# Optimization experiments

Measured on AMD Instinct MI355X. Metric: run time of the kernel, lower is better.

## Reference

```python
import jax, jax.numpy as jnp
import numpy as np

D_MODEL = 512; D_STATE = 128; D_CONV = 4; EXPAND = 2; HEADDIM = 64; CHUNK = 64
D_INNER = EXPAND * D_MODEL            # 1024
NHEADS = D_INNER // HEADDIM           # 16
CONV_DIM = D_INNER + 2 * D_STATE      # 1280
D_IN_PROJ = 2 * D_INNER + 2 * D_STATE + NHEADS  # 2320
BATCH, SEQLEN = 2, 8192


def setup_inputs() -> dict:
    key = jax.random.key(0)
    ks = jax.random.split(key, 8)
    s = 0.02
    return {
        "x": jax.random.normal(ks[0], (BATCH, SEQLEN, D_MODEL), jnp.float32),
        "in_proj_w": jax.random.normal(ks[1], (D_IN_PROJ, D_MODEL), jnp.float32) * s,
        "conv_w": jax.random.normal(ks[2], (CONV_DIM, 1, D_CONV), jnp.float32) * s,
        "conv_b": jnp.zeros((CONV_DIM,), jnp.float32),
        "dt_bias": jax.random.normal(ks[3], (NHEADS,), jnp.float32) * s,
        "A_log": jnp.log(jnp.arange(1, NHEADS + 1, dtype=jnp.float32)),
        "D_skip": jnp.ones((NHEADS,), jnp.float32),
        "norm_w": jnp.ones((D_INNER,), jnp.float32),
        "ssm_out_w": jax.random.normal(ks[4], (D_MODEL, D_INNER), jnp.float32) * s,
        "fuse_w": jax.random.normal(ks[5], (D_MODEL, 2 * D_MODEL), jnp.float32) * s,
        "fuse_b": jnp.zeros((D_MODEL,), jnp.float32),
    }


def segsum(a):
    # a: (..., T) -> (..., T, T) with [i, j] = sum_{j < d <= i} a[d]; -inf above diag
    T = a.shape[-1]
    a = jnp.broadcast_to(a[..., :, None], a.shape + (T,))
    a = jnp.where(jnp.tril(jnp.ones((T, T), bool), -1), a, 0.0)
    a = jnp.cumsum(a, axis=-2)
    return jnp.where(jnp.tril(jnp.ones((T, T), bool), 0), a, -jnp.inf)


def ssd(x, A, B, C):
    # x: (b,l,h,p), A: (b,l,h), B/C: (b,l,n) (single group, broadcast over heads)
    b, l, h, p = x.shape
    c = l // CHUNK
    x = x.reshape(b, c, CHUNK, h, p)
    A = jnp.transpose(A.reshape(b, c, CHUNK, h), (0, 3, 1, 2))   # (b,h,c,s)
    B = B.reshape(b, c, CHUNK, -1)
    C = C.reshape(b, c, CHUNK, -1)
    A_cumsum = jnp.cumsum(A, axis=-1)                             # (b,h,c,s)
    L = jnp.exp(segsum(A))                                        # (b,h,c,s,s) intra-chunk decay
    Y_diag = jnp.einsum("bcln,bcsn,bhcls,bcshp->bclhp", C, B, L, x)
    decay_states = jnp.exp(A_cumsum[..., -1:] - A_cumsum)         # (b,h,c,s)
    states = jnp.einsum("bcln,bhcl,bclhp->bchpn", B, decay_states, x)
    init = jnp.zeros_like(states[:, :1])
    A_pad = jnp.pad(A_cumsum[..., -1], ((0, 0), (0, 0), (1, 0)))  # (b,h,c+1)
    decay_chunk = jnp.exp(segsum(A_pad))                          # (b,h,c+1,c+1)
    new_states = jnp.einsum("bhzc,bchpn->bzhpn", decay_chunk,
                            jnp.concatenate([init, states], axis=1))
    states = new_states[:, :-1]                                   # state entering each chunk
    state_decay_out = jnp.exp(A_cumsum)
    Y_off = jnp.einsum("bchpn,bcsn,bhcs->bcshp", states, C, state_decay_out)
    return (Y_diag + Y_off).reshape(b, l, h, p)


def mamba2_block(u, in_proj_w, conv_w, conv_b, dt_bias, A_log, D_skip, norm_w, ssm_out_w):
    b, l, _ = u.shape
    zxbcdt = u @ in_proj_w.T                                      # (b,l,2320)
    z = zxbcdt[..., :D_INNER]
    xBC = zxbcdt[..., D_INNER:D_INNER + CONV_DIM]
    dt = jax.nn.softplus(zxbcdt[..., -NHEADS:] + dt_bias)         # (b,l,h)
    # depthwise causal conv over time
    conv = jax.lax.conv_general_dilated(
        jnp.transpose(xBC, (0, 2, 1)), conv_w, (1,), [(D_CONV - 1, 0)],
        dimension_numbers=("NCH", "OIH", "NCH"), feature_group_count=CONV_DIM)
    xBC = jax.nn.silu(jnp.transpose(conv + conv_b[None, :, None], (0, 2, 1)))
    xh = xBC[..., :D_INNER].reshape(b, l, NHEADS, HEADDIM)
    Bm = xBC[..., D_INNER:D_INNER + D_STATE]
    Cm = xBC[..., -D_STATE:]
    A = -jnp.exp(A_log)                                           # (h,)
    y = ssd(xh * dt[..., None], A * dt, Bm, Cm)
    y = y + xh * D_skip[None, None, :, None]
    y = y.reshape(b, l, D_INNER)
    # gated RMSNorm
    y = y * jax.nn.silu(z)
    y = y * jax.lax.rsqrt(jnp.mean(y * y, axis=-1, keepdims=True) + 1e-5) * norm_w
    return y @ ssm_out_w.T


def reference(x, in_proj_w, conv_w, conv_b, dt_bias, A_log, D_skip, norm_w,
              ssm_out_w, fuse_w, fuse_b):
    args = (in_proj_w, conv_w, conv_b, dt_bias, A_log, D_skip, norm_w, ssm_out_w)
    y_fwd = mamba2_block(x, *args)
    y_rev = jnp.flip(mamba2_block(jnp.flip(x, 1), *args), 1)
    y_cat = jnp.concatenate([y_fwd, y_rev], axis=-1)
    return y_cat @ fuse_w.T + fuse_b
```

## Files before the change

### kernel.cpp

```cpp
#include <hip/hip_runtime.h>
#include <cstddef>

#define B_SZ     2
#define L_SEQ    8192
#define D_INNERC 1024
#define NHEADSC  16
#define CHUNKC   64
#define NCHUNKC  128
#define CONV_DIMC 1280
#define D_PROJC  2320
#define M_ROWS   16384

typedef unsigned short bfu;

using bf16x8 = __attribute__((ext_vector_type(8))) short;
using f32x4  = __attribute__((ext_vector_type(4))) float;

__device__ __forceinline__ float silu_(float v) { return v / (1.f + expf(-v)); }

__device__ __forceinline__ float b2f(bfu u) {
  return __uint_as_float((unsigned)u << 16);
}
__device__ __forceinline__ bfu f2b(float f) {
  unsigned x = __float_as_uint(f);
  return (bfu)((x + 0x7fffu + ((x >> 16) & 1u)) >> 16);
}

__device__ __forceinline__ float4 ld4(const float* p) { return *(const float4*)p; }
__device__ __forceinline__ float4 ld4(const bfu* p) {
  ushort4 u = *(const ushort4*)p;
  float4 f;
  f.x = b2f(u.x); f.y = b2f(u.y); f.z = b2f(u.z); f.w = b2f(u.w);
  return f;
}
__device__ __forceinline__ void st4(float* p, float4 v) { *(float4*)p = v; }
__device__ __forceinline__ void st4(bfu* p, float4 v) {
  ushort4 u;
  u.x = f2b(v.x); u.y = f2b(v.y); u.z = f2b(v.z); u.w = f2b(v.w);
  *(ushort4*)p = u;
}

__device__ __forceinline__ void gl_lds16(const bfu* g, bfu* l) {
  __builtin_amdgcn_global_load_lds(
      (const __attribute__((address_space(1))) unsigned int*)g,
      (__attribute__((address_space(3))) unsigned int*)l, 16, 0, 0);
}

__device__ __forceinline__ int pos_of(int b, int c, int l, int dir) {
  int t = c * CHUNKC + l;
  return dir ? (b * L_SEQ + (L_SEQ - 1) - t) : (b * L_SEQ + t);
}

__global__ __launch_bounds__(256)
void mfma_nt(const bfu* __restrict__ A, int lda,
             const bfu* __restrict__ Bw, int ldb,
             void* __restrict__ Cv, int ldc,
             int N, int K, const float* __restrict__ bias, int mode)
{
  __shared__ bfu sh[16384];
  bfu* As = sh;
  bfu* Bs = sh + 8192;
  const int tid  = threadIdx.x;
  const int lane = tid & 63;
  const int wave = __builtin_amdgcn_readfirstlane(tid >> 6);
  const int wm = wave & 1, wn = wave >> 1;

  const int num_n = gridDim.x;
  const int flat  = blockIdx.y * num_n + blockIdx.x;
  const int xcd   = flat & 7;
  const int g     = flat >> 3;
  const int n0 = (g % num_n) * 128;
  const int m0 = ((g / num_n) * 8 + xcd) * 128;

  f32x4 acc[4][4];
#pragma unroll
  for (int i = 0; i < 4; ++i)
#pragma unroll
    for (int j = 0; j < 4; ++j)
      acc[i][j] = (f32x4){0.f, 0.f, 0.f, 0.f};

  const int ro   = lane >> 3;
  const int slot = lane & 7;

  for (int k0 = 0; k0 < K; k0 += 64) {
    __syncthreads();
#pragma unroll
    for (int si = 0; si < 4; ++si) {
      int r = wave * 32 + si * 8 + ro;
      int cg = slot ^ (r & 7);
      gl_lds16(A  + (size_t)(m0 + r) * lda + k0 + cg * 8, As + (wave * 32 + si * 8) * 64);
      gl_lds16(Bw + (size_t)(n0 + r) * ldb + k0 + cg * 8, Bs + (wave * 32 + si * 8) * 64);
    }
    __syncthreads();

#pragma unroll
    for (int ks = 0; ks < 2; ++ks) {
      bf16x8 af[4], bfr[4];
#pragma unroll
      for (int i = 0; i < 4; ++i) {
        int ra = wm * 64 + i * 16 + (lane & 15);
        int ca = (ks * 4 + (lane >> 4)) ^ (ra & 7);
        af[i] = *(const bf16x8*)(As + ra * 64 + ca * 8);
        int rb = wn * 64 + i * 16 + (lane & 15);
        int cb = (ks * 4 + (lane >> 4)) ^ (rb & 7);
        bfr[i] = *(const bf16x8*)(Bs + rb * 64 + cb * 8);
      }
#pragma unroll
      for (int i = 0; i < 4; ++i)
#pragma unroll
        for (int j = 0; j < 4; ++j)
          acc[i][j] = __builtin_amdgcn_mfma_f32_16x16x32_bf16(af[i], bfr[j], acc[i][j], 0, 0, 0);
    }
  }

  __syncthreads();
  if (mode == 0) {
#pragma unroll
    for (int i = 0; i < 4; ++i)
#pragma unroll
      for (int j = 0; j < 4; ++j)
#pragma unroll
        for (int r = 0; r < 4; ++r) {
          int ml = wm * 64 + i * 16 + (lane >> 4) * 4 + r;
          int nl = wn * 64 + j * 16 + (lane & 15);
          sh[ml * 128 + nl] = f2b(acc[i][j][r]);
        }
    __syncthreads();
    bfu* Cb = (bfu*)Cv;
#pragma unroll
    for (int rr = 0; rr < 8; ++rr) {
      int idx = rr * 256 + tid;
      int row = idx >> 4, co = (idx & 15) * 8;
      if (n0 + co < N) {
        *(ulonglong2*)(Cb + (size_t)(m0 + row) * ldc + n0 + co) =
            *(const ulonglong2*)(sh + row * 128 + co);
      }
    }
  } else {
    float* Cf = (float*)Cv;
    float* shf = (float*)sh;
#pragma unroll
    for (int p = 0; p < 2; ++p) {
      if (wm == p) {
#pragma unroll
        for (int i = 0; i < 4; ++i)
#pragma unroll
          for (int j = 0; j < 4; ++j)
#pragma unroll
            for (int r = 0; r < 4; ++r) {
              int ml = i * 16 + (lane >> 4) * 4 + r;
              int nl = wn * 64 + j * 16 + (lane & 15);
              shf[ml * 128 + nl] = acc[i][j][r];
            }
      }
      __syncthreads();
#pragma unroll
      for (int rr = 0; rr < 8; ++rr) {
        int idx = rr * 256 + tid;
        int row = idx >> 5, co = (idx & 31) * 4;
        int n = n0 + co;
        if (n < N) {
          float4 v = *(float4*)(shf + row * 128 + co);
          float* cp = Cf + (size_t)(m0 + p * 64 + row) * ldc + n;
          if (mode == 2) {
            float4 o = *(float4*)cp;
            v.x += o.x; v.y += o.y; v.z += o.z; v.w += o.w;
          } else if (bias) {
            v.x += bias[n]; v.y += bias[n + 1]; v.z += bias[n + 2]; v.w += bias[n + 3];
          }
          *(float4*)cp = v;
        }
      }
      __syncthreads();
    }
  }
}

__global__ __launch_bounds__(512)
void mfma_nt_8p(const bfu* __restrict__ A, int lda,
                const bfu* __restrict__ Bw, int ldb,
                bfu* __restrict__ C, int ldc, int N, int K)
{
  __shared__ bfu sh[65536];
  bfu* As0 = sh;
  bfu* As1 = sh + 16384;
  bfu* Bs0 = sh + 32768;
  bfu* Bs1 = sh + 49152;

  const int tid  = threadIdx.x;
  const int lane = tid & 63;
  const int w    = __builtin_amdgcn_readfirstlane(tid >> 6);
  const int wm = w & 1, wn = w >> 1;
  const int q = lane >> 4, t = lane & 15;

  const int num_n = gridDim.x;
  const int flat  = blockIdx.y * num_n + blockIdx.x;
  const int xcd   = flat & 7;
  const int g     = flat >> 3;
  const int n0 = (g % num_n) * 256;
  const int m0 = ((g / num_n) * 8 + xcd) * 256;

  auto STG = [&](const bfu* __restrict__ X, int ldx, int x0, int kt, int h,
                 bfu* dst) {
#pragma unroll
    for (int ci = 0; ci < 2; ++ci) {
      int rb = h * 128 + ci * 64 + w * 8;
      int r  = rb + (lane >> 3);
      int cg = (lane & 7) ^ (r & 7);
      gl_lds16(X + (size_t)(x0 + r) * ldx + kt * 64 + cg * 8, dst + rb * 64);
    }
  };
  auto FR = [&](const bfu* tile, int R, int gg) -> bf16x8 {
    return *(const bf16x8*)(tile + R * 64 + ((gg ^ (R & 7)) * 8));
  };

  f32x4 acc[8][4];
#pragma unroll
  for (int i = 0; i < 8; ++i)
#pragma unroll
    for (int j = 0; j < 4; ++j)
      acc[i][j] = (f32x4){0.f, 0.f, 0.f, 0.f};

  STG(Bw, ldb, n0, 0, 0, Bs0); STG(Bw, ldb, n0, 0, 1, Bs0);
  STG(A,  lda, m0, 0, 0, As0); STG(A,  lda, m0, 0, 1, As0);
  STG(Bw, ldb, n0, 1, 0, Bs1); STG(Bw, ldb, n0, 1, 1, Bs1);
  asm volatile("s_waitcnt vmcnt(4)" ::: "memory");
  __builtin_amdgcn_s_barrier();

  const int nIter = K >> 7;
  bf16x8 bfr[4][2];
  for (int it = 0; it < nIter; ++it) {
    const int kt = it * 2;
    const bool last = (it == nIter - 1);

#pragma unroll
    for (int p = 0; p < 4; ++p) {
      bf16x8 af[2][2];
#pragma unroll
      for (int ii = 0; ii < 2; ++ii)
#pragma unroll
        for (int ks = 0; ks < 2; ++ks)
          af[ii][ks] = FR(As0, wm * 128 + (2 * p + ii) * 16 + t, ks * 4 + q);
      if (p == 0) {
#pragma unroll
        for (int j = 0; j < 4; ++j)
#pragma unroll
          for (int ks = 0; ks < 2; ++ks)
            bfr[j][ks] = FR(Bs0, wn * 64 + j * 16 + t, ks * 4 + q);
      }
      if (p == 0)          STG(A,  lda, m0, kt + 1, 0, As1);
      if (p == 1)          STG(A,  lda, m0, kt + 1, 1, As1);
      if (p == 2 && !last) STG(Bw, ldb, n0, kt + 2, 0, Bs0);
      if (p == 3 && !last) STG(Bw, ldb, n0, kt + 2, 1, Bs0);
      if (p == 3) {
        if (last) asm volatile("s_waitcnt vmcnt(0)" ::: "memory");
        else      asm volatile("s_waitcnt vmcnt(4)" ::: "memory");
      }
      __builtin_amdgcn_s_barrier();
      __builtin_amdgcn_s_setprio(1);
#pragma unroll
      for (int ks = 0; ks < 2; ++ks)
#pragma unroll
        for (int ii = 0; ii < 2; ++ii)
#pragma unroll
          for (int j = 0; j < 4; ++j)
            acc[2 * p + ii][j] = __builtin_amdgcn_mfma_f32_16x16x32_bf16(
                af[ii][ks], bfr[j][ks], acc[2 * p + ii][j], 0, 0, 0);
      __builtin_amdgcn_s_setprio(0);
      __builtin_amdgcn_s_barrier();
    }

#pragma unroll
    for (int p = 0; p < 4; ++p) {
      bf16x8 af[2][2];
#pragma unroll
      for (int ii = 0; ii < 2; ++ii)
#pragma unroll
        for (int ks = 0; ks < 2; ++ks)
          af[ii][ks] = FR(As1, wm * 128 + (2 * p + ii) * 16 + t, ks * 4 + q);
      if (p == 0) {
#pragma unroll
        for (int j = 0; j < 4; ++j)
#pragma unroll
          for (int ks = 0; ks < 2; ++ks)
            bfr[j][ks] = FR(Bs1, wn * 64 + j * 16 + t, ks * 4 + q);
      }
      if (p == 0 && !last) STG(A,  lda, m0, kt + 2, 0, As0);
      if (p == 1 && !last) STG(A,  lda, m0, kt + 2, 1, As0);
      if (p == 2 && !last) STG(Bw, ldb, n0, kt + 3, 0, Bs1);
      if (p == 3 && !last) STG(Bw, ldb, n0, kt + 3, 1, Bs1);
      if (p == 3 && !last) asm volatile("s_waitcnt vmcnt(4)" ::: "memory");
      __builtin_amdgcn_s_barrier();
      __builtin_amdgcn_s_setprio(1);
#pragma unroll
      for (int ks = 0; ks < 2; ++ks)
#pragma unroll
        for (int ii = 0; ii < 2; ++ii)
#pragma unroll
          for (int j = 0; j < 4; ++j)
            acc[2 * p + ii][j] = __builtin_amdgcn_mfma_f32_16x16x32_bf16(
                af[ii][ks], bfr[j][ks], acc[2 * p + ii][j], 0, 0, 0);
      __builtin_amdgcn_s_setprio(0);
      __builtin_amdgcn_s_barrier();
    }
  }

#pragma unroll
  for (int i = 0; i < 8; ++i)
#pragma unroll
    for (int j = 0; j < 4; ++j)
#pragma unroll
      for (int r = 0; r < 4; ++r) {
        int ml = wm * 128 + i * 16 + q * 4 + r;
        int nl = wn * 64 + j * 16 + t;
        sh[ml * 256 + nl] = f2b(acc[i][j][r]);
      }
  __syncthreads();
#pragma unroll
  for (int rr = 0; rr < 16; ++rr) {
    int idx = rr * 512 + tid;
    int row = idx >> 5, co = (idx & 31) * 8;
    if (n0 + co < N) {
      *(ulonglong2*)(C + (size_t)(m0 + row) * ldc + n0 + co) =
          *(const ulonglong2*)(sh + row * 256 + co);
    }
  }
}

__global__ __launch_bounds__(256)
void cvt_x_k(const float* __restrict__ in, bfu* __restrict__ out)
{
  int q = blockIdx.x * 256 + threadIdx.x;
  st4(out + (size_t)q * 4, ld4(in + (size_t)q * 4));
}

__global__ __launch_bounds__(256)
void cvt_w_k(const float* __restrict__ in, bfu* __restrict__ out)
{
  int q = blockIdx.x * 256 + threadIdx.x;
  int row = q >> 7, c4 = (q & 127) << 2;
  float4 v = {0.f, 0.f, 0.f, 0.f};
  if (row < D_PROJC) v = ld4(in + (size_t)row * 512 + c4);
  st4(out + (size_t)row * 512 + c4, v);
}

__global__ __launch_bounds__(256)
void transpose_k(const float* __restrict__ in, bfu* __restrict__ out)
{
  int idx = blockIdx.x * 256 + threadIdx.x;
  int j = idx >> 9, k = idx & 511;
  out[idx] = f2b(in[k * 1024 + j]);
}

__global__ __launch_bounds__(256)
void cvt_fuse_k(const float* __restrict__ in, bfu* __restrict__ out)
{
  int q = blockIdx.x * 256 + threadIdx.x;
  int m = q >> 7, kg = (q & 127) << 2;
  float4 v = ld4(in + (size_t)(m & 511) * 1024 + (m >> 9) * 512 + kg);
  st4(out + (size_t)m * 512 + kg, v);
}

__global__ __launch_bounds__(256)
void conv_k(const bfu* __restrict__ zx, const float* __restrict__ conv_w,
            const float* __restrict__ conv_b, bfu* __restrict__ xBC, int dir)
{
  int ch = blockIdx.x * 256 + threadIdx.x;
  int m0 = blockIdx.y * 8;
  int b  = m0 >> 13, tb = m0 & (L_SEQ - 1);
  float w0 = conv_w[ch * 4 + 0], w1 = conv_w[ch * 4 + 1];
  float w2 = conv_w[ch * 4 + 2], w3 = conv_w[ch * 4 + 3];
  float cb = conv_b[ch];
  const bfu* src = zx + 1024 + ch;
  const int shift = dir ? 0 : 3;

  float v[11];
#pragma unroll
  for (int i = 0; i < 11; ++i) {
    int tt = tb + i - shift;
    v[i] = (tt >= 0 && tt < L_SEQ)
         ? b2f(src[(size_t)(b * L_SEQ + tt) * D_PROJC]) : 0.f;
  }
#pragma unroll
  for (int j = 0; j < 8; ++j) {
    float acc = cb;
    if (dir == 0) {
      acc += w0 * v[j] + w1 * v[j + 1] + w2 * v[j + 2] + w3 * v[j + 3];
    } else {
      acc += w0 * v[j + 3] + w1 * v[j + 2] + w2 * v[j + 1] + w3 * v[j];
    }
    xBC[(size_t)(m0 + j) * CONV_DIMC + ch] = f2b(silu_(acc));
  }
}

__global__ __launch_bounds__(256)
void states_mfma_k(const bfu* __restrict__ zx, const bfu* __restrict__ xBC,
                   const float* __restrict__ dt_bias, const float* __restrict__ A_log,
                   float* __restrict__ acum_g, float* __restrict__ dt_g,
                   bfu* __restrict__ states, int dir)
{
  __shared__ bfu BT[128 * 72];
  __shared__ bfu xsT[64 * 72];
  __shared__ float scaleS[8 * 64];

  int bid = blockIdx.x;
  int hb = bid >> 8;
  int c = bid & 127, b = (bid >> 7) & 1;
  int tid = threadIdx.x, lane = tid & 63;
  int w = tid >> 6, q = lane >> 4, t = lane & 15;

#pragma unroll
  for (int rr = 0; rr < 2; ++rr) {
    int i = w + rr * 4;
    int h = hb * 8 + i;
    int l = lane;
    int pos = pos_of(b, c, l, dir);
    float dtr = b2f(zx[(size_t)pos * D_PROJC + 2304 + h]) + dt_bias[h];
    float dt = (dtr > 20.f) ? dtr : log1pf(expf(dtr));
    float a = -expf(A_log[h]) * dt;
#pragma unroll
    for (int off = 1; off < 64; off <<= 1) {
      float v = __shfl_up(a, off);
      if (l >= off) a += v;
    }
    float alast = __shfl(a, 63);
    int gi = ((b * NCHUNKC + c) * NHEADSC + h) * 64 + l;
    acum_g[gi] = a; dt_g[gi] = dt;
    scaleS[i * 64 + l] = dt * expf(alast - a);
  }

#pragma unroll
  for (int r = 0; r < 8; ++r) {
    int qq = tid + r * 256;
    int l = qq & 63, ng = qq >> 6;
    ushort4 v = *(const ushort4*)(xBC + (size_t)pos_of(b, c, l, dir) * CONV_DIMC + 1024 + ng * 4);
    BT[(ng * 4 + 0) * 72 + l] = v.x; BT[(ng * 4 + 1) * 72 + l] = v.y;
    BT[(ng * 4 + 2) * 72 + l] = v.z; BT[(ng * 4 + 3) * 72 + l] = v.w;
  }
  __syncthreads();

  for (int i = 0; i < 8; ++i) {
    int h = hb * 8 + i;
#pragma unroll
    for (int r = 0; r < 4; ++r) {
      int qq = tid + r * 256;
      int l = qq & 63, pg = qq >> 6;
      float s = scaleS[i * 64 + l];
      ushort4 v = *(const ushort4*)(xBC + (size_t)pos_of(b, c, l, dir) * CONV_DIMC + h * 64 + pg * 4);
      xsT[(pg * 4 + 0) * 72 + l] = f2b(b2f(v.x) * s);
      xsT[(pg * 4 + 1) * 72 + l] = f2b(b2f(v.y) * s);
      xsT[(pg * 4 + 2) * 72 + l] = f2b(b2f(v.z) * s);
      xsT[(pg * 4 + 3) * 72 + l] = f2b(b2f(v.w) * s);
    }
    __syncthreads();

    bf16x8 axs[2];
#pragma unroll
    for (int ks = 0; ks < 2; ++ks)
      axs[ks] = *(const bf16x8*)(xsT + (w * 16 + t) * 72 + ks * 32 + q * 8);

    f32x4 acc[8];
#pragma unroll
    for (int j = 0; j < 8; ++j) acc[j] = (f32x4){0.f, 0.f, 0.f, 0.f};
#pragma unroll
    for (int ks = 0; ks < 2; ++ks)
#pragma unroll
      for (int j = 0; j < 8; ++j) {
        bf16x8 bB = *(const bf16x8*)(BT + (j * 16 + t) * 72 + ks * 32 + q * 8);
        acc[j] = __builtin_amdgcn_mfma_f32_16x16x32_bf16(axs[ks], bB, acc[j], 0, 0, 0);
      }

    size_t base = ((size_t)(b * NCHUNKC + c) * NHEADSC + h) * 8192;
#pragma unroll
    for (int j = 0; j < 8; ++j)
#pragma unroll
      for (int r = 0; r < 4; ++r) {
        int p = w * 16 + q * 4 + r, n = j * 16 + t;
        states[base + p * 128 + n] = f2b(acc[j][r]);
      }
    __syncthreads();
  }
}

__global__ __launch_bounds__(256)
void scan_k(bfu* __restrict__ states, const float* __restrict__ acum_g)
{
  int bid = blockIdx.x;
  int eb = bid & 15, h = (bid >> 4) & 15, b = bid >> 8;
  int e = eb * 512 + threadIdx.x * 2;
  bfu* p0 = states + ((size_t)(b * NCHUNKC) * NHEADSC + h) * 8192 + e;
  const float* ac = acum_g + ((b * NCHUNKC) * NHEADSC + h) * 64 + 63;
  const size_t cstride = (size_t)NHEADSC * 8192;
  const int astride = NHEADSC * 64;

  float pre0 = 0.f, pre1 = 0.f;
  uint raw = *(const uint*)p0;
  float dcur = expf(ac[0]);
  for (int c = 0; c < NCHUNKC; ++c) {
    uint raw_next = 0; float dnext = 0.f;
    if (c < NCHUNKC - 1) {
      raw_next = *(const uint*)(p0 + (c + 1) * cstride);
      dnext = expf(ac[(c + 1) * astride]);
    }
    float v0 = b2f((bfu)(raw & 0xffff));
    float v1 = b2f((bfu)(raw >> 16));
    uint packed = (uint)f2b(pre0) | ((uint)f2b(pre1) << 16);
    *(uint*)(p0 + c * cstride) = packed;
    pre0 = v0 + dcur * pre0;
    pre1 = v1 + dcur * pre1;
    raw = raw_next; dcur = dnext;
  }
}

__global__ __launch_bounds__(256)
void y_mfma_k(const bfu* __restrict__ xBC, const bfu* __restrict__ states,
              const float* __restrict__ acum_g, const float* __restrict__ dt_g,
              const float* __restrict__ D_skip, bfu* __restrict__ ybuf, int dir)
{
  __shared__ bfu smem[30976];
  bfu* Cs  = smem;
  bfu* Bsc = smem + 8704;
  bfu* Ps  = smem + 17408;
  bfu* xhT = smem + 26112;
  float* acumH = (float*)(smem + 30720);
  float* dtH   = acumH + 64;

  int bid = blockIdx.x;
  int hb = bid >> 8;
  int c = bid & 127, b = (bid >> 7) & 1;
  int tid = threadIdx.x, lane = tid & 63;
  int w = tid >> 6, q = lane >> 4, t = lane & 15;

#pragma unroll
  for (int r = 0; r < 8; ++r) {
    int qq = tid + r * 256;
    int row = qq >> 5, grp = qq & 31;
    const bfu* src = xBC + (size_t)pos_of(b, c, row, dir) * CONV_DIMC;
    *(ushort4*)(Cs  + row * 136 + grp * 4) = *(const ushort4*)(src + 1152 + grp * 4);
    *(ushort4*)(Bsc + row * 136 + grp * 4) = *(const ushort4*)(src + 1024 + grp * 4);
  }
  __syncthreads();

  bf16x8 af[4];
#pragma unroll
  for (int ks = 0; ks < 4; ++ks)
    af[ks] = *(const bf16x8*)(Cs + (w * 16 + t) * 136 + ks * 32 + q * 8);

  f32x4 sacc[4];
#pragma unroll
  for (int j = 0; j < 4; ++j) sacc[j] = (f32x4){0.f, 0.f, 0.f, 0.f};
#pragma unroll
  for (int ks = 0; ks < 4; ++ks)
#pragma unroll
    for (int j = 0; j < 4; ++j) {
      bf16x8 bf = *(const bf16x8*)(Bsc + (j * 16 + t) * 136 + ks * 32 + q * 8);
      sacc[j] = __builtin_amdgcn_mfma_f32_16x16x32_bf16(af[ks], bf, sacc[j], 0, 0, 0);
    }

  for (int i = 0; i < 8; ++i) {
    int h = hb * 8 + i;
    __syncthreads();
    size_t pbase = ((size_t)(b * NCHUNKC + c) * NHEADSC + h) * 8192;
#pragma unroll
    for (int r = 0; r < 8; ++r) {
      int qq = tid + r * 256;
      int row = qq >> 5, grp = qq & 31;
      *(ushort4*)(Ps + row * 136 + grp * 4) =
          *(const ushort4*)(states + pbase + row * 128 + grp * 4);
    }
#pragma unroll
    for (int r = 0; r < 4; ++r) {
      int qq = tid + r * 256;
      int l = qq & 63, pg = qq >> 6;
      ushort4 v = *(const ushort4*)(xBC + (size_t)pos_of(b, c, l, dir) * CONV_DIMC + h * 64 + pg * 4);
      xhT[(pg * 4 + 0) * 72 + l] = v.x; xhT[(pg * 4 + 1) * 72 + l] = v.y;
      xhT[(pg * 4 + 2) * 72 + l] = v.z; xhT[(pg * 4 + 3) * 72 + l] = v.w;
    }
    if (tid < 64) {
      int gi = ((b * NCHUNKC + c) * NHEADSC + h) * 64 + tid;
      acumH[tid] = acum_g[gi]; dtH[tid] = dt_g[gi];
    }
    __syncthreads();

    f32x4 yacc[4];
#pragma unroll
    for (int j = 0; j < 4; ++j) yacc[j] = (f32x4){0.f, 0.f, 0.f, 0.f};
#pragma unroll
    for (int ks = 0; ks < 4; ++ks)
#pragma unroll
      for (int j = 0; j < 4; ++j) {
        bf16x8 bP = *(const bf16x8*)(Ps + (j * 16 + t) * 136 + ks * 32 + q * 8);
        yacc[j] = __builtin_amdgcn_mfma_f32_16x16x32_bf16(af[ks], bP, yacc[j], 0, 0, 0);
      }

    float Dh = D_skip[h];
    bfu* sc = Bsc;
#pragma unroll
    for (int j = 0; j < 4; ++j)
#pragma unroll
      for (int r = 0; r < 4; ++r) {
        int l = w * 16 + q * 4 + r, s = j * 16 + t;
        float v = 0.f;
        if (s <= l) v = sacc[j][r] * expf(acumH[l] - acumH[s]) * dtH[s];
        if (s == l) v += Dh;
        sc[l * 72 + s] = f2b(v);
      }

    f32x4 acc2[4];
    float dec[4];
#pragma unroll
    for (int r = 0; r < 4; ++r) dec[r] = expf(acumH[w * 16 + q * 4 + r]);
#pragma unroll
    for (int j = 0; j < 4; ++j)
#pragma unroll
      for (int r = 0; r < 4; ++r) acc2[j][r] = yacc[j][r] * dec[r];

#pragma unroll
    for (int ks = 0; ks < 2; ++ks) {
      bf16x8 asc = *(const bf16x8*)(sc + (w * 16 + t) * 72 + ks * 32 + q * 8);
#pragma unroll
      for (int j = 0; j < 4; ++j) {
        bf16x8 bx = *(const bf16x8*)(xhT + (j * 16 + t) * 72 + ks * 32 + q * 8);
        acc2[j] = __builtin_amdgcn_mfma_f32_16x16x32_bf16(asc, bx, acc2[j], 0, 0, 0);
      }
    }

#pragma unroll
    for (int j = 0; j < 4; ++j)
#pragma unroll
      for (int r = 0; r < 4; ++r) {
        int l = w * 16 + q * 4 + r, p = j * 16 + t;
        ybuf[(size_t)pos_of(b, c, l, dir) * D_INNERC + h * 64 + p] = f2b(acc2[j][r]);
      }
  }
}

__global__ __launch_bounds__(256)
void norm_k(bfu* __restrict__ ybuf, const bfu* __restrict__ zx,
            const float* __restrict__ norm_w)
{
  int m = blockIdx.x, tid = threadIdx.x;
  float4 y = ld4(ybuf + (size_t)m * D_INNERC + tid * 4);
  float4 z = ld4(zx + (size_t)m * D_PROJC + tid * 4);
  float4 g;
  g.x = y.x * silu_(z.x); g.y = y.y * silu_(z.y);
  g.z = y.z * silu_(z.z); g.w = y.w * silu_(z.w);
  float ss = g.x * g.x + g.y * g.y + g.z * g.z + g.w * g.w;
#pragma unroll
  for (int off = 32; off >= 1; off >>= 1) ss += __shfl_xor(ss, off);
  __shared__ float red[4];
  int wid = tid >> 6;
  if ((tid & 63) == 0) red[wid] = ss;
  __syncthreads();
  float tot = red[0] + red[1] + red[2] + red[3];
  float scale = rsqrtf(tot * (1.f / 1024.f) + 1e-5f);
  float4 w = *(const float4*)(norm_w + tid * 4);
  g.x *= scale * w.x; g.y *= scale * w.y; g.z *= scale * w.z; g.w *= scale * w.w;
  st4(ybuf + (size_t)m * D_INNERC + tid * 4, g);
}

extern "C" void kernel_launch(void* const* d_in, const int* in_sizes, int n_in,
                              void* d_out, int out_size, void* d_ws, size_t ws_size,
                              hipStream_t stream)
{
  const float* x         = (const float*)d_in[0];
  const float* in_proj_w = (const float*)d_in[1];
  const float* conv_w    = (const float*)d_in[2];
  const float* conv_b    = (const float*)d_in[3];
  const float* dt_bias   = (const float*)d_in[4];
  const float* A_log     = (const float*)d_in[5];
  const float* D_skip    = (const float*)d_in[6];
  const float* norm_w    = (const float*)d_in[7];
  const float* ssm_out_w = (const float*)d_in[8];
  const float* fuse_w    = (const float*)d_in[9];
  const float* fuse_b    = (const float*)d_in[10];
  float* out = (float*)d_out;

  bfu* zx     = (bfu*)d_ws;
  bfu* xBC    = zx     + (size_t)M_ROWS * D_PROJC;
  bfu* states = xBC    + (size_t)M_ROWS * CONV_DIMC;
  bfu* ybuf   = states + (size_t)33554432;
  float* acum = (float*)(ybuf + (size_t)M_ROWS * D_INNERC);
  float* dtg  = acum + 262144;
  bfu* ssmTb  = (bfu*)(dtg + 262144);
  bfu* fuseA  = ssmTb + 524288;
  bfu* wcmb   = fuseA + 524288;
  bfu* xb = states;
  bfu* wb = states + 8388608;

  cvt_x_k<<<8192, 256, 0, stream>>>(x, xb);
  cvt_w_k<<<1280, 256, 0, stream>>>(in_proj_w, wb);
  transpose_k<<<2048, 256, 0, stream>>>(ssm_out_w, ssmTb);
  cvt_fuse_k<<<512, 256, 0, stream>>>(fuse_w, fuseA);

  mfma_nt<<<dim3(8, 8), 256, 0, stream>>>(
      fuseA, 512, ssmTb, 512, wcmb, 1024, 1024, 512, nullptr, 0);

  mfma_nt_8p<<<dim3(10, 64), 512, 0, stream>>>(
      xb, 512, wb, 512, zx, D_PROJC, D_PROJC, 512);

  for (int dir = 0; dir < 2; ++dir) {
    conv_k<<<dim3(5, 2048), 256, 0, stream>>>(zx, conv_w, conv_b, xBC, dir);
    states_mfma_k<<<512, 256, 0, stream>>>(zx, xBC, dt_bias, A_log, acum, dtg, states, dir);
    scan_k<<<512, 256, 0, stream>>>(states, acum);
    y_mfma_k<<<512, 256, 0, stream>>>(xBC, states, acum, dtg, D_skip, ybuf, dir);
    norm_k<<<M_ROWS, 256, 0, stream>>>(ybuf, zx, norm_w);
    mfma_nt<<<dim3(4, 128), 256, 0, stream>>>(
        ybuf, 1024, wcmb + (size_t)dir * 524288, 1024, out, 512,
        512, 1024, dir == 0 ? fuse_b : nullptr, dir == 0 ? 1 : 2);
  }
}
```

Baseline: 530.0 us.

## Double-buffer GEMM LDS tiles and prefetch next-head loads in SSD kernels

New measurement: 548.6 us. +3.5%, slower.

```diff
diff --git a/kernel.cpp b/kernel.cpp
--- a/kernel.cpp
+++ b/kernel.cpp
@@ -57,9 +57,7 @@
              void* __restrict__ Cv, int ldc,
              int N, int K, const float* __restrict__ bias, int mode)
 {
-  __shared__ bfu sh[16384];
-  bfu* As = sh;
-  bfu* Bs = sh + 8192;
+  __shared__ bfu sh[32768];
   const int tid  = threadIdx.x;
   const int lane = tid & 63;
   const int wave = __builtin_amdgcn_readfirstlane(tid >> 6);
@@ -82,16 +80,28 @@
   const int ro   = lane >> 3;
   const int slot = lane & 7;
 
-  for (int k0 = 0; k0 < K; k0 += 64) {
-    __syncthreads();
+  auto STAGE = [&](int k0, int buf) {
+    bfu* Asb = sh + buf * 16384;
+    bfu* Bsb = Asb + 8192;
 #pragma unroll
     for (int si = 0; si < 4; ++si) {
       int r = wave * 32 + si * 8 + ro;
       int cg = slot ^ (r & 7);
-      gl_lds16(A  + (size_t)(m0 + r) * lda + k0 + cg * 8, As + (wave * 32 + si * 8) * 64);
-      gl_lds16(Bw + (size_t)(n0 + r) * ldb + k0 + cg * 8, Bs + (wave * 32 + si * 8) * 64);
-    }
-    __syncthreads();
+      gl_lds16(A  + (size_t)(m0 + r) * lda + k0 + cg * 8, Asb + (wave * 32 + si * 8) * 64);
+      gl_lds16(Bw + (size_t)(n0 + r) * ldb + k0 + cg * 8, Bsb + (wave * 32 + si * 8) * 64);
+    }
+  };
+
+  STAGE(0, 0);
+  asm volatile("s_waitcnt vmcnt(0)" ::: "memory");
+  __builtin_amdgcn_s_barrier();
+
+  const int nk = K >> 6;
+  for (int kt = 0; kt < nk; ++kt) {
+    const int cur = kt & 1;
+    if (kt + 1 < nk) STAGE((kt + 1) << 6, cur ^ 1);
+    const bfu* As = sh + cur * 16384;
+    const bfu* Bs = As + 8192;
 
 #pragma unroll
     for (int ks = 0; ks < 2; ++ks) {
@@ -111,6 +121,8 @@
         for (int j = 0; j < 4; ++j)
           acc[i][j] = __builtin_amdgcn_mfma_f32_16x16x32_bf16(af[i], bfr[j], acc[i][j], 0, 0, 0);
     }
+    asm volatile("s_waitcnt vmcnt(0)" ::: "memory");
+    __builtin_amdgcn_s_barrier();
   }
 
   __syncthreads();
@@ -437,6 +449,18 @@
     BT[(ng * 4 + 0) * 72 + l] = v.x; BT[(ng * 4 + 1) * 72 + l] = v.y;
     BT[(ng * 4 + 2) * 72 + l] = v.z; BT[(ng * 4 + 3) * 72 + l] = v.w;
   }
+
+  ushort4 xr[4];
+  auto PREFX = [&](int i) {
+    int h = hb * 8 + i;
+#pragma unroll
+    for (int r = 0; r < 4; ++r) {
+      int qq = tid + r * 256;
+      int l = qq & 63, pg = qq >> 6;
+      xr[r] = *(const ushort4*)(xBC + (size_t)pos_of(b, c, l, dir) * CONV_DIMC + h * 64 + pg * 4);
+    }
+  };
+  PREFX(0);
   __syncthreads();
 
   for (int i = 0; i < 8; ++i) {
@@ -446,12 +470,13 @@
       int qq = tid + r * 256;
       int l = qq & 63, pg = qq >> 6;
       float s = scaleS[i * 64 + l];
-      ushort4 v = *(const ushort4*)(xBC + (size_t)pos_of(b, c, l, dir) * CONV_DIMC + h * 64 + pg * 4);
+      ushort4 v = xr[r];
       xsT[(pg * 4 + 0) * 72 + l] = f2b(b2f(v.x) * s);
       xsT[(pg * 4 + 1) * 72 + l] = f2b(b2f(v.y) * s);
       xsT[(pg * 4 + 2) * 72 + l] = f2b(b2f(v.z) * s);
       xsT[(pg * 4 + 3) * 72 + l] = f2b(b2f(v.w) * s);
     }
+    if (i < 7) PREFX(i + 1);
     __syncthreads();
 
     bf16x8 axs[2];
@@ -482,33 +507,51 @@
   }
 }
 
+#define SCAN_STEP(RW, DD, CI)                                                 \
+  {                                                                           \
+    unsigned long long raw_ = RW; float dc_ = DD;                             \
+    if ((CI) + 4 < NCHUNKC) {                                                 \
+      RW = *(const unsigned long long*)(p0 + (size_t)((CI) + 4) * cstride);   \
+      DD = expf(ac[((CI) + 4) * astride]);                                    \
+    }                                                                         \
+    unsigned long long pk =                                                   \
+        (unsigned long long)f2b(pre0) |                                       \
+        ((unsigned long long)f2b(pre1) << 16) |                               \
+        ((unsigned long long)f2b(pre2) << 32) |                               \
+        ((unsigned long long)f2b(pre3) << 48);                                \
+    *(unsigned long long*)(p0 + (size_t)(CI) * cstride) = pk;                 \
+    pre0 = b2f((bfu)raw_) + dc_ * pre0;                                       \
+    pre1 = b2f((bfu)(raw_ >> 16)) + dc_ * pre1;                               \
+    pre2 = b2f((bfu)(raw_ >> 32)) + dc_ * pre2;                               \
+    pre3 = b2f((bfu)(raw_ >> 48)) + dc_ * pre3;                               \
+  }
+
 __global__ __launch_bounds__(256)
 void scan_k(bfu* __restrict__ states, const float* __restrict__ acum_g)
 {
   int bid = blockIdx.x;
-  int eb = bid & 15, h = (bid >> 4) & 15, b = bid >> 8;
-  int e = eb * 512 + threadIdx.x * 2;
+  int eb = bid & 7, h = (bid >> 3) & 15, b = bid >> 7;
+  int e = eb * 1024 + threadIdx.x * 4;
   bfu* p0 = states + ((size_t)(b * NCHUNKC) * NHEADSC + h) * 8192 + e;
   const float* ac = acum_g + ((b * NCHUNKC) * NHEADSC + h) * 64 + 63;
   const size_t cstride = (size_t)NHEADSC * 8192;
   const int astride = NHEADSC * 64;
 
-  float pre0 = 0.f, pre1 = 0.f;
-  uint raw = *(const uint*)p0;
-  float dcur = expf(ac[0]);
-  for (int c = 0; c < NCHUNKC; ++c) {
-    uint raw_next = 0; float dnext = 0.f;
-    if (c < NCHUNKC - 1) {
-      raw_next = *(const uint*)(p0 + (c + 1) * cstride);
-      dnext = expf(ac[(c + 1) * astride]);
-    }
-    float v0 = b2f((bfu)(raw & 0xffff));
-    float v1 = b2f((bfu)(raw >> 16));
-    uint packed = (uint)f2b(pre0) | ((uint)f2b(pre1) << 16);
-    *(uint*)(p0 + c * cstride) = packed;
-    pre0 = v0 + dcur * pre0;
-    pre1 = v1 + dcur * pre1;
-    raw = raw_next; dcur = dnext;
+  float pre0 = 0.f, pre1 = 0.f, pre2 = 0.f, pre3 = 0.f;
+  unsigned long long r0 = *(const unsigned long long*)(p0);
+  unsigned long long r1 = *(const unsigned long long*)(p0 + cstride);
+  unsigned long long r2 = *(const unsigned long long*)(p0 + 2 * cstride);
+  unsigned long long r3 = *(const unsigned long long*)(p0 + 3 * cstride);
+  float d0 = expf(ac[0]);
+  float d1 = expf(ac[astride]);
+  float d2 = expf(ac[2 * astride]);
+  float d3 = expf(ac[3 * astride]);
+
+  for (int c = 0; c < NCHUNKC; c += 4) {
+    SCAN_STEP(r0, d0, c);
+    SCAN_STEP(r1, d1, c + 1);
+    SCAN_STEP(r2, d2, c + 2);
+    SCAN_STEP(r3, d3, c + 3);
   }
 }
 
@@ -539,6 +582,31 @@
     *(ushort4*)(Cs  + row * 136 + grp * 4) = *(const ushort4*)(src + 1152 + grp * 4);
     *(ushort4*)(Bsc + row * 136 + grp * 4) = *(const ushort4*)(src + 1024 + grp * 4);
   }
+
+  ushort4 psr[8], xhr[4];
+  float aR = 0.f, dR = 0.f;
+  size_t base0 = ((size_t)(b * NCHUNKC + c) * NHEADSC + hb * 8) * 8192;
+  auto PREF = [&](int i) {
+    int h = hb * 8 + i;
+    size_t pbase = base0 + (size_t)i * 8192;
+#pragma unroll
+    for (int r = 0; r < 8; ++r) {
+      int qq = tid + r * 256;
+      int row = qq >> 5, grp = qq & 31;
+      psr[r] = *(const ushort4*)(states + pbase + row * 128 + grp * 4);
+    }
+#pragma unroll
+    for (int r = 0; r < 4; ++r) {
+      int qq = tid + r * 256;
+      int l = qq & 63, pg = qq >> 6;
+      xhr[r] = *(const ushort4*)(xBC + (size_t)pos_of(b, c, l, dir) * CONV_DIMC + h * 64 + pg * 4);
+    }
+    if (tid < 64) {
+      int gi = ((b * NCHUNKC + c) * NHEADSC + h) * 64 + tid;
+      aR = acum_g[gi]; dR = dt_g[gi];
+    }
+  };
+  PREF(0);
   __syncthreads();
 
   bf16x8 af[4];
@@ -560,26 +628,22 @@
   for (int i = 0; i < 8; ++i) {
     int h = hb * 8 + i;
     __syncthreads();
-    size_t pbase = ((size_t)(b * NCHUNKC + c) * NHEADSC + h) * 8192;
 #pragma unroll
     for (int r = 0; r < 8; ++r) {
       int qq = tid + r * 256;
       int row = qq >> 5, grp = qq & 31;
-      *(ushort4*)(Ps + row * 136 + grp * 4) =
-          *(const ushort4*)(states + pbase + row * 128 + grp * 4);
+      *(ushort4*)(Ps + row * 136 + grp * 4) = psr[r];
     }
 #pragma unroll
     for (int r = 0; r < 4; ++r) {
       int qq = tid + r * 256;
       int l = qq & 63, pg = qq >> 6;
-      ushort4 v = *(const ushort4*)(xBC + (size_t)pos_of(b, c, l, dir) * CONV_DIMC + h * 64 + pg * 4);
+      ushort4 v = xhr[r];
       xhT[(pg * 4 + 0) * 72 + l] = v.x; xhT[(pg * 4 + 1) * 72 + l] = v.y;
       xhT[(pg * 4 + 2) * 72 + l] = v.z; xhT[(pg * 4 + 3) * 72 + l] = v.w;
     }
-    if (tid < 64) {
-      int gi = ((b * NCHUNKC + c) * NHEADSC + h) * 64 + tid;
-      acumH[tid] = acum_g[gi]; dtH[tid] = dt_g[gi];
-    }
+    if (tid < 64) { acumH[tid] = aR; dtH[tid] = dR; }
+    if (i < 7) PREF(i + 1);
     __syncthreads();
 
     f32x4 yacc[4];
@@ -702,7 +766,7 @@
   for (int dir = 0; dir < 2; ++dir) {
     conv_k<<<dim3(5, 2048), 256, 0, stream>>>(zx, conv_w, conv_b, xBC, dir);
     states_mfma_k<<<512, 256, 0, stream>>>(zx, xBC, dt_bias, A_log, acum, dtg, states, dir);
-    scan_k<<<512, 256, 0, stream>>>(states, acum);
+    scan_k<<<256, 256, 0, stream>>>(states, acum);
     y_mfma_k<<<512, 256, 0, stream>>>(xBC, states, acum, dtg, D_skip, ybuf, dir);
     norm_k<<<M_ROWS, 256, 0, stream>>>(ybuf, zx, norm_w);
     mfma_nt<<<dim3(4, 128), 256, 0, stream>>>(
```
